# Kernel tuning notes

Hardware: AMD Instinct MI355X
Metric: run time of the kernel (lower is better)

## Reference

```python
import jax, jax.numpy as jnp
import numpy as np

B, N, D = 8, 256, 128
EPS_AGG = 1e-6
LN_EPS = 1e-5


def setup_inputs() -> dict:
    key = jax.random.key(0)
    ks = jax.random.split(key, 12)
    s = lambda fan_in: 1.0 / np.sqrt(fan_in)
    inp = {
        "x": jax.random.normal(ks[0], (B, N, D), dtype=jnp.float32),
        "edge0": jax.random.normal(ks[1], (B, N, N, D), dtype=jnp.float32),
        "edge_mask": jax.random.randint(ks[2], (B, N, N), 0, 2, dtype=jnp.int32),
        # msg_mlp: Linear(3D->D), ReLU, Linear(D->D)
        "W1m": jax.random.uniform(ks[3], (3 * D, D), jnp.float32, -s(3 * D), s(3 * D)),
        "b1m": jax.random.uniform(ks[4], (D,), jnp.float32, -s(3 * D), s(3 * D)),
        "W2m": jax.random.uniform(ks[5], (D, D), jnp.float32, -s(D), s(D)),
        "b2m": jax.random.uniform(ks[6], (D,), jnp.float32, -s(D), s(D)),
        # upd_mlp: Linear(2D->D), ReLU, Linear(D->D)
        "W1u": jax.random.uniform(ks[7], (2 * D, D), jnp.float32, -s(2 * D), s(2 * D)),
        "b1u": jax.random.uniform(ks[8], (D,), jnp.float32, -s(2 * D), s(2 * D)),
        "W2u": jax.random.uniform(ks[9], (D, D), jnp.float32, -s(D), s(D)),
        "b2u": jax.random.uniform(ks[10], (D,), jnp.float32, -s(D), s(D)),
        # LayerNorm affine
        "gamma": jnp.ones((D,), jnp.float32),
        "beta": jnp.zeros((D,), jnp.float32),
    }
    return inp


def reference(x, edge0, edge_mask, W1m, b1m, W2m, b2m, W1u, b1u, W2u, b2u, gamma, beta):
    # All-pairs concat: [B, N_i, N_j, 3D]
    xi = jnp.broadcast_to(x[:, :, None, :], (B, N, N, D))
    xj = jnp.broadcast_to(x[:, None, :, :], (B, N, N, D))
    msg_in = jnp.concatenate([xi, xj, edge0], axis=-1)
    # 2-layer edge MLP
    h = jax.nn.relu(jnp.einsum("bijk,kd->bijd", msg_in, W1m) + b1m)
    msg = jnp.einsum("bijk,kd->bijd", h, W2m) + b2m
    # mask + mean-style aggregation over neighbors j
    m = edge_mask.astype(jnp.float32)
    agg = jnp.einsum("bijd,bij->bid", msg, m) / (m.sum(axis=2, keepdims=True) + EPS_AGG)
    # update MLP
    u_in = jnp.concatenate([x, agg], axis=-1)  # [B, N, 2D]
    hu = jax.nn.relu(u_in @ W1u + b1u)
    out = hu @ W2u + b2u
    # residual + LayerNorm
    y = x + out
    mu = y.mean(axis=-1, keepdims=True)
    var = y.var(axis=-1, keepdims=True)
    return (y - mu) * jax.lax.rsqrt(var + LN_EPS) * gamma + beta
```

## Files before the change

kernel.cpp:

```cpp
#include <hip/hip_runtime.h>
#include <hip/hip_bf16.h>

typedef float    f4    __attribute__((ext_vector_type(4)));
typedef short    s8v   __attribute__((ext_vector_type(8)));
typedef __bf16   bf8v  __attribute__((ext_vector_type(8)));
typedef unsigned int u32x4v __attribute__((ext_vector_type(4)));
typedef unsigned short u16;

typedef const __attribute__((address_space(1))) void GAS;
typedef __attribute__((address_space(3))) void LAS;

#define NB 8
#define NN 256
#define ND 128

static __device__ __forceinline__ u16 f2bf(float f) {
    union { float f; unsigned u; } v; v.f = f;
    unsigned r = v.u + 0x7FFF + ((v.u >> 16) & 1);
    return (u16)(r >> 16);
}

static __device__ __forceinline__ unsigned pack2bf(float a, float b) {
    unsigned ua = __builtin_bit_cast(unsigned, a) + 0x8000u;
    unsigned ub = __builtin_bit_cast(unsigned, b) + 0x8000u;
    return __builtin_amdgcn_perm(ub, ua, 0x07060302u);
}

__global__ __launch_bounds__(256) void prep_kernel(
    const float* __restrict__ x, const float* __restrict__ W1m,
    const float* __restrict__ b1m,
    float* __restrict__ P, float* __restrict__ Qn, u16* __restrict__ W1cp)
{
    if (blockIdx.x == 1024) {
        for (int idx = threadIdx.x; idx < 16384; idx += 256) {
            int e  = idx & 7;
            int ln = (idx >> 3) & 63;
            int nt = (idx >> 9) & 7;
            int kt = idx >> 12;
            int k  = kt * 32 + (ln >> 4) * 8 + e;
            int d  = nt * 16 + (ln & 15);
            W1cp[idx] = f2bf(W1m[(2 * ND + k) * ND + d]);
        }
        return;
    }
    __shared__ float xl[256];
    int t = threadIdx.x;
    int row0 = blockIdx.x * 2;
    xl[t] = x[row0 * ND + t];
    __syncthreads();
    int r = t >> 7;
    int d = t & 127;
    int row = row0 + r;
    float sp = b1m[d], sq = 0.f;
    const float* xr = &xl[r * ND];
    #pragma unroll 8
    for (int k = 0; k < ND; ++k) {
        float xv = xr[k];
        sp += xv * W1m[k * ND + d];
        sq += xv * W1m[(ND + k) * ND + d];
    }
    P[row * ND + d] = sp;
    Qn[row * ND + d] = sq;
}

__global__ __launch_bounds__(256, 5) void fused_kernel(
    const float* __restrict__ x, const float* __restrict__ edge0,
    const int* __restrict__ mask,
    const float* __restrict__ W2m, const float* __restrict__ b2m,
    const float* __restrict__ W1u, const float* __restrict__ b1u,
    const float* __restrict__ W2u, const float* __restrict__ b2u,
    const float* __restrict__ gamma, const float* __restrict__ beta,
    const float* __restrict__ P, const float* __restrict__ Qn,
    const u16* __restrict__ W1cp,
    float* __restrict__ out)
{
    __shared__ float ebuf[3][2048];
    __shared__ float ml[NN];
    __shared__ float xrow[ND];
    __shared__ float redc[4], redA[4], redB[4];

    float* aggH = &ebuf[1][0];
    float* am   = &ebuf[1][128];
    float* hu   = &ebuf[1][256];
    float* yl   = &ebuf[1][384];

    const int bid  = (blockIdx.x & 7) * 256 + (blockIdx.x >> 3);
    const int b    = bid >> 8;
    const int tid  = threadIdx.x;
    const int wave = tid >> 6;
    const int lane = tid & 63;
    const int l15  = lane & 15;
    const int lg   = lane >> 4;

    const char* e0c = (const char*)(edge0 + (size_t)bid * (NN * ND));

    float mval = (float)mask[bid * NN + tid];
    ml[tid] = mval;
    if (tid < ND) xrow[tid] = x[bid * ND + tid];

    s8v bfr[4][2];
    #pragma unroll
    for (int kt = 0; kt < 4; ++kt)
        #pragma unroll
        for (int n = 0; n < 2; ++n)
            bfr[kt][n] = *reinterpret_cast<const s8v*>(
                &W1cp[(((kt * 8) + (wave * 2 + n)) * 64 + lane) * 8]);

    const int col0 = wave * 32 + l15;
    const float pv0 = P[bid * ND + col0];
    const float pv1 = P[bid * ND + col0 + 16];
    const float* qbase = Qn + ((size_t)b * NN + lg * 4) * ND + col0;

    auto STAGE = [&](int cc, int bb) {
        const char* cb = e0c + (size_t)cc * 8192;
        #pragma unroll
        for (int u = 0; u < 2; ++u) {
            int row  = wave * 4 + u * 2 + (lane >> 5);
            int colb = (lane & 31) * 16;
            const char* g = cb + row * 512 + (colb ^ ((row & 7) << 4));
            __builtin_amdgcn_global_load_lds(
                (GAS*)g, (LAS*)&ebuf[bb][(wave * 2 + u) * 256], 16, 0, 0);
        }
    };

    float q0v[2][4], q1v[2][4];
    auto LOADQ = [&](int cc, int gg) {
        const float* qr = qbase + (size_t)cc * 16 * ND;
        #pragma unroll
        for (int r = 0; r < 4; ++r) {
            q0v[gg][r] = qr[r * ND];
            q1v[gg][r] = qr[r * ND + 16];
        }
    };

    float agg0 = 0.f, agg1 = 0.f;

    asm volatile("s_waitcnt vmcnt(0) lgkmcnt(0)" ::: "memory");
    __builtin_amdgcn_sched_barrier(0);
    STAGE(0, 0);
    __builtin_amdgcn_sched_barrier(0);
    LOADQ(0, 0);
    __builtin_amdgcn_sched_barrier(0);
    STAGE(1, 1);
    __builtin_amdgcn_sched_barrier(0);

    #pragma unroll
    for (int c = 0; c < 16; ++c) {
        if (c < 15)
            asm volatile("s_waitcnt vmcnt(10) lgkmcnt(0)" ::: "memory");
        else
            asm volatile("s_waitcnt vmcnt(8) lgkmcnt(0)" ::: "memory");
        __builtin_amdgcn_s_barrier();
        __builtin_amdgcn_sched_barrier(0);
        if (c < 15) {
            LOADQ(c + 1, (c + 1) & 1);
            __builtin_amdgcn_sched_barrier(0);
            if (c < 14) {
                STAGE(c + 2, (c + 2) % 3);
                __builtin_amdgcn_sched_barrier(0);
            }
        }
        const char* bufc = (const char*)&ebuf[c % 3][0];
        const int rb  = l15 * 512;
        const int swz = (l15 & 7) << 4;
        f4 acc0 = {0.f, 0.f, 0.f, 0.f};
        f4 acc1 = {0.f, 0.f, 0.f, 0.f};
        #pragma unroll
        for (int kt = 0; kt < 4; ++kt) {
            int cbyte = kt * 128 + lg * 32;
            f4 a0 = *reinterpret_cast<const f4*>(bufc + rb + ((cbyte)      ^ swz));
            f4 a1 = *reinterpret_cast<const f4*>(bufc + rb + ((cbyte + 16) ^ swz));
            u32x4v aw;
            aw[0] = pack2bf(a0[0], a0[1]);
            aw[1] = pack2bf(a0[2], a0[3]);
            aw[2] = pack2bf(a1[0], a1[1]);
            aw[3] = pack2bf(a1[2], a1[3]);
            bf8v av = __builtin_bit_cast(bf8v, aw);
            acc0 = __builtin_amdgcn_mfma_f32_16x16x32_bf16(
                av, __builtin_bit_cast(bf8v, bfr[kt][0]), acc0, 0, 0, 0);
            acc1 = __builtin_amdgcn_mfma_f32_16x16x32_bf16(
                av, __builtin_bit_cast(bf8v, bfr[kt][1]), acc1, 0, 0, 0);
        }
        f4 mk = *reinterpret_cast<const f4*>(&ml[c * 16 + lg * 4]);
        const int g = c & 1;
        #pragma unroll
        for (int r = 0; r < 4; ++r) {
            float h0 = fmaxf(acc0[r] + pv0 + q0v[g][r], 0.f);
            float h1 = fmaxf(acc1[r] + pv1 + q1v[g][r], 0.f);
            agg0 += mk[r] * h0;
            agg1 += mk[r] * h1;
        }
    }

    agg0 += __shfl_xor(agg0, 16); agg0 += __shfl_xor(agg0, 32);
    agg1 += __shfl_xor(agg1, 16); agg1 += __shfl_xor(agg1, 32);
    if (lg == 0) {
        aggH[wave * 32 + l15]      = agg0;
        aggH[wave * 32 + 16 + l15] = agg1;
    }
    float cv = mval;
    #pragma unroll
    for (int o = 32; o > 0; o >>= 1) cv += __shfl_xor(cv, o);
    if (lane == 0) redc[wave] = cv;
    __syncthreads();

    const float cnt = redc[0] + redc[1] + redc[2] + redc[3];
    const float inv = 1.f / (cnt + 1e-6f);
    const int d  = tid & 127;
    const int hf = tid >> 7;

    {
        float s = 0.f;
        #pragma unroll 8
        for (int k = hf * 64; k < hf * 64 + 64; ++k) s += aggH[k] * W2m[k * ND + d];
        ml[tid] = s;
    }
    __syncthreads();
    if (tid < ND) am[d] = (ml[d] + ml[d + ND] + cnt * b2m[d]) * inv;
    __syncthreads();
    {
        float s = 0.f;
        const float* W = W1u + (size_t)hf * ND * ND;
        const float* v = hf ? am : xrow;
        #pragma unroll 8
        for (int k = 0; k < ND; ++k) s += v[k] * W[k * ND + d];
        ml[tid] = s;
    }
    __syncthreads();
    if (tid < ND) hu[d] = fmaxf(ml[d] + ml[d + ND] + b1u[d], 0.f);
    __syncthreads();
    {
        float s = 0.f;
        #pragma unroll 8
        for (int k = hf * 64; k < hf * 64 + 64; ++k) s += hu[k] * W2u[k * ND + d];
        ml[tid] = s;
    }
    __syncthreads();
    if (tid < ND) yl[d] = xrow[d] + ml[d] + ml[d + ND] + b2u[d];
    __syncthreads();
    float yv = (tid < ND) ? yl[tid] : 0.f;
    float s1 = yv, s2 = yv * yv;
    #pragma unroll
    for (int o = 32; o > 0; o >>= 1) { s1 += __shfl_xor(s1, o); s2 += __shfl_xor(s2, o); }
    if (lane == 0) { redA[wave] = s1; redB[wave] = s2; }
    __syncthreads();
    if (tid < ND) {
        float mu  = (redA[0] + redA[1] + redA[2] + redA[3]) * (1.f / 128.f);
        float ex2 = (redB[0] + redB[1] + redB[2] + redB[3]) * (1.f / 128.f);
        float var = ex2 - mu * mu;
        float rs  = rsqrtf(var + 1e-5f);
        out[bid * ND + d] = (yl[d] - mu) * rs * gamma[d] + beta[d];
    }
}

extern "C" void kernel_launch(void* const* d_in, const int* in_sizes, int n_in,
                              void* d_out, int out_size, void* d_ws, size_t ws_size,
                              hipStream_t stream) {
    (void)in_sizes; (void)n_in; (void)out_size; (void)ws_size;
    const float* x     = (const float*)d_in[0];
    const float* edge0 = (const float*)d_in[1];
    const int*   mask  = (const int*)d_in[2];
    const float* W1m   = (const float*)d_in[3];
    const float* b1m   = (const float*)d_in[4];
    const float* W2m   = (const float*)d_in[5];
    const float* b2m   = (const float*)d_in[6];
    const float* W1u   = (const float*)d_in[7];
    const float* b1u   = (const float*)d_in[8];
    const float* W2u   = (const float*)d_in[9];
    const float* b2u   = (const float*)d_in[10];
    const float* gamma = (const float*)d_in[11];
    const float* beta  = (const float*)d_in[12];

    float* P    = (float*)d_ws;
    float* Qn   = P + 2048 * 128;
    u16*   W1cp = (u16*)(Qn + 2048 * 128);

    float* o = (float*)d_out;

    prep_kernel<<<dim3(1025), dim3(256), 0, stream>>>(x, W1m, b1m, P, Qn, W1cp);
    fused_kernel<<<dim3(2048), dim3(256), 0, stream>>>(
        x, edge0, mask, W2m, b2m, W1u, b1u, W2u, b2u, gamma, beta,
        P, Qn, W1cp, o);
}
```

Measured before the change: 95.60 us.

## Stage edge tiles through registers and store them as bf16 in LDS

Measured after the change: 82.11 us. 14.1% less time.

```diff
diff --git a/kernel.cpp b/kernel.cpp
--- a/kernel.cpp
+++ b/kernel.cpp
@@ -6,9 +6,6 @@
 typedef __bf16   bf8v  __attribute__((ext_vector_type(8)));
 typedef unsigned int u32x4v __attribute__((ext_vector_type(4)));
 typedef unsigned short u16;
-
-typedef const __attribute__((address_space(1))) void GAS;
-typedef __attribute__((address_space(3))) void LAS;
 
 #define NB 8
 #define NN 256
@@ -74,7 +71,7 @@
     const u16* __restrict__ W1cp,
     float* __restrict__ out)
 {
-    __shared__ float ebuf[3][2048];
+    __shared__ float ebuf[3][1024];
     __shared__ float ml[NN];
     __shared__ float xrow[ND];
     __shared__ float redc[4], redA[4], redB[4];
@@ -111,97 +108,95 @@
     const float pv1 = P[bid * ND + col0 + 16];
     const float* qbase = Qn + ((size_t)b * NN + lg * 4) * ND + col0;
 
-    auto STAGE = [&](int cc, int bb) {
-        const char* cb = e0c + (size_t)cc * 8192;
-        #pragma unroll
-        for (int u = 0; u < 2; ++u) {
-            int row  = wave * 4 + u * 2 + (lane >> 5);
-            int colb = (lane & 31) * 16;
-            const char* g = cb + row * 512 + (colb ^ ((row & 7) << 4));
-            __builtin_amdgcn_global_load_lds(
-                (GAS*)g, (LAS*)&ebuf[bb][(wave * 2 + u) * 256], 16, 0, 0);
-        }
+    const int srow  = tid >> 4;
+    const int swoff = srow * 256 + (((tid & 15) * 16) ^ ((srow & 7) << 4));
+
+    auto LOADE = [&](int cc, f4* er) {
+        const char* cb = e0c + (size_t)cc * 8192 + tid * 32;
+        er[0] = *reinterpret_cast<const f4*>(cb);
+        er[1] = *reinterpret_cast<const f4*>(cb + 16);
     };
-
-    float q0v[2][4], q1v[2][4];
-    auto LOADQ = [&](int cc, int gg) {
-        const float* qr = qbase + (size_t)cc * 16 * ND;
-        #pragma unroll
-        for (int r = 0; r < 4; ++r) {
-            q0v[gg][r] = qr[r * ND];
-            q1v[gg][r] = qr[r * ND + 16];
-        }
+    auto WRITEE = [&](const f4* er, int bb) {
+        u32x4v aw;
+        aw[0] = pack2bf(er[0][0], er[0][1]);
+        aw[1] = pack2bf(er[0][2], er[0][3]);
+        aw[2] = pack2bf(er[1][0], er[1][1]);
+        aw[3] = pack2bf(er[1][2], er[1][3]);
+        *reinterpret_cast<u32x4v*>(
+            reinterpret_cast<char*>(&ebuf[bb][0]) + swoff) = aw;
     };
 
     float agg0 = 0.f, agg1 = 0.f;
-
-    asm volatile("s_waitcnt vmcnt(0) lgkmcnt(0)" ::: "memory");
+    f4 eA[2], eB[2];
+
+    LOADE(0, eA);
     __builtin_amdgcn_sched_barrier(0);
-    STAGE(0, 0);
+    LOADE(1, eB);
     __builtin_amdgcn_sched_barrier(0);
-    LOADQ(0, 0);
-    __builtin_amdgcn_sched_barrier(0);
-    STAGE(1, 1);
-    __builtin_amdgcn_sched_barrier(0);
+    asm volatile("s_waitcnt vmcnt(2)" ::: "memory");
+    WRITEE(eA, 0);
+    asm volatile("s_waitcnt lgkmcnt(0)" ::: "memory");
 
     #pragma unroll
     for (int c = 0; c < 16; ++c) {
-        if (c < 15)
-            asm volatile("s_waitcnt vmcnt(10) lgkmcnt(0)" ::: "memory");
-        else
-            asm volatile("s_waitcnt vmcnt(8) lgkmcnt(0)" ::: "memory");
         __builtin_amdgcn_s_barrier();
         __builtin_amdgcn_sched_barrier(0);
-        if (c < 15) {
-            LOADQ(c + 1, (c + 1) & 1);
+        float q0v[4], q1v[4];
+        {
+            const float* qr = qbase + (size_t)c * 16 * ND;
+            #pragma unroll
+            for (int r = 0; r < 4; ++r) {
+                q0v[r] = qr[r * ND];
+                q1v[r] = qr[r * ND + 16];
+            }
+        }
+        __builtin_amdgcn_sched_barrier(0);
+        if (c < 14) {
+            if (c & 1) LOADE(c + 2, eA); else LOADE(c + 2, eB);
             __builtin_amdgcn_sched_barrier(0);
-            if (c < 14) {
-                STAGE(c + 2, (c + 2) % 3);
-                __builtin_amdgcn_sched_barrier(0);
-            }
         }
         const char* bufc = (const char*)&ebuf[c % 3][0];
-        const int rb  = l15 * 512;
+        const int rb  = l15 * 256;
         const int swz = (l15 & 7) << 4;
         f4 acc0 = {0.f, 0.f, 0.f, 0.f};
         f4 acc1 = {0.f, 0.f, 0.f, 0.f};
         #pragma unroll
         for (int kt = 0; kt < 4; ++kt) {
-            int cbyte = kt * 128 + lg * 32;
-            f4 a0 = *reinterpret_cast<const f4*>(bufc + rb + ((cbyte)      ^ swz));
-            f4 a1 = *reinterpret_cast<const f4*>(bufc + rb + ((cbyte + 16) ^ swz));
-            u32x4v aw;
-            aw[0] = pack2bf(a0[0], a0[1]);
-            aw[1] = pack2bf(a0[2], a0[3]);
-            aw[2] = pack2bf(a1[0], a1[1]);
-            aw[3] = pack2bf(a1[2], a1[3]);
-            bf8v av = __builtin_bit_cast(bf8v, aw);
+            s8v av = *reinterpret_cast<const s8v*>(
+                bufc + rb + ((kt * 64 + lg * 16) ^ swz));
             acc0 = __builtin_amdgcn_mfma_f32_16x16x32_bf16(
-                av, __builtin_bit_cast(bf8v, bfr[kt][0]), acc0, 0, 0, 0);
+                __builtin_bit_cast(bf8v, av), __builtin_bit_cast(bf8v, bfr[kt][0]), acc0, 0, 0, 0);
             acc1 = __builtin_amdgcn_mfma_f32_16x16x32_bf16(
-                av, __builtin_bit_cast(bf8v, bfr[kt][1]), acc1, 0, 0, 0);
+                __builtin_bit_cast(bf8v, av), __builtin_bit_cast(bf8v, bfr[kt][1]), acc1, 0, 0, 0);
         }
         f4 mk = *reinterpret_cast<const f4*>(&ml[c * 16 + lg * 4]);
-        const int g = c & 1;
         #pragma unroll
         for (int r = 0; r < 4; ++r) {
-            float h0 = fmaxf(acc0[r] + pv0 + q0v[g][r], 0.f);
-            float h1 = fmaxf(acc1[r] + pv1 + q1v[g][r], 0.f);
+            float h0 = fmaxf(acc0[r] + pv0 + q0v[r], 0.f);
+            float h1 = fmaxf(acc1[r] + pv1 + q1v[r], 0.f);
             agg0 += mk[r] * h0;
             agg1 += mk[r] * h1;
         }
+        __builtin_amdgcn_sched_barrier(0);
+        if (c < 15) {
+            asm volatile("s_waitcnt vmcnt(2)" ::: "memory");
+            if (c & 1) WRITEE(eA, (c + 1) % 3); else WRITEE(eB, (c + 1) % 3);
+            asm volatile("s_waitcnt lgkmcnt(0)" ::: "memory");
+            __builtin_amdgcn_sched_barrier(0);
+        }
     }
 
     agg0 += __shfl_xor(agg0, 16); agg0 += __shfl_xor(agg0, 32);
     agg1 += __shfl_xor(agg1, 16); agg1 += __shfl_xor(agg1, 32);
+    float cv = mval;
+    #pragma unroll
+    for (int o = 32; o > 0; o >>= 1) cv += __shfl_xor(cv, o);
+    if (lane == 0) redc[wave] = cv;
+    __syncthreads();
     if (lg == 0) {
         aggH[wave * 32 + l15]      = agg0;
         aggH[wave * 32 + 16 + l15] = agg1;
     }
-    float cv = mval;
-    #pragma unroll
-    for (int o = 32; o > 0; o >>= 1) cv += __shfl_xor(cv, o);
-    if (lane == 0) redc[wave] = cv;
     __syncthreads();
 
     const float cnt = redc[0] + redc[1] + redc[2] + redc[3];
```

## Split fused kernel into per-wave edge kernel and batched node tail kernel

Applied to the files above, without the earlier changes.

After: 128.9 us. 1.35x slower.

```diff
diff --git a/kernel.cpp b/kernel.cpp
--- a/kernel.cpp
+++ b/kernel.cpp
@@ -5,6 +5,7 @@
 typedef short    s8v   __attribute__((ext_vector_type(8)));
 typedef __bf16   bf8v  __attribute__((ext_vector_type(8)));
 typedef unsigned int u32x4v __attribute__((ext_vector_type(4)));
+typedef int      i4    __attribute__((ext_vector_type(4)));
 typedef unsigned short u16;
 
 typedef const __attribute__((address_space(1))) void GAS;
@@ -13,6 +14,7 @@
 #define NB 8
 #define NN 256
 #define ND 128
+#define SB0() __builtin_amdgcn_sched_barrier(0)
 
 static __device__ __forceinline__ u16 f2bf(float f) {
     union { float f; unsigned u; } v; v.f = f;
@@ -29,7 +31,7 @@
 __global__ __launch_bounds__(256) void prep_kernel(
     const float* __restrict__ x, const float* __restrict__ W1m,
     const float* __restrict__ b1m,
-    float* __restrict__ P, float* __restrict__ Qn, u16* __restrict__ W1cp)
+    float* __restrict__ P, float* __restrict__ Qp2, u16* __restrict__ W1cp)
 {
     if (blockIdx.x == 1024) {
         for (int idx = threadIdx.x; idx < 16384; idx += 256) {
@@ -48,11 +50,11 @@
     int row0 = blockIdx.x * 2;
     xl[t] = x[row0 * ND + t];
     __syncthreads();
-    int r = t >> 7;
+    int r2 = t >> 7;
     int d = t & 127;
-    int row = row0 + r;
+    int row = row0 + r2;
     float sp = b1m[d], sq = 0.f;
-    const float* xr = &xl[r * ND];
+    const float* xr = &xl[r2 * ND];
     #pragma unroll 8
     for (int k = 0; k < ND; ++k) {
         float xv = xr[k];
@@ -60,43 +62,36 @@
         sq += xv * W1m[(ND + k) * ND + d];
     }
     P[row * ND + d] = sp;
-    Qn[row * ND + d] = sq;
-}
-
-__global__ __launch_bounds__(256, 5) void fused_kernel(
-    const float* __restrict__ x, const float* __restrict__ edge0,
-    const int* __restrict__ mask,
-    const float* __restrict__ W2m, const float* __restrict__ b2m,
-    const float* __restrict__ W1u, const float* __restrict__ b1u,
-    const float* __restrict__ W2u, const float* __restrict__ b2u,
-    const float* __restrict__ gamma, const float* __restrict__ beta,
-    const float* __restrict__ P, const float* __restrict__ Qn,
+    int b   = row >> 8;
+    int j   = row & 255;
+    int gc  = j >> 4;
+    int lgq = (j & 15) >> 2;
+    int r   = j & 3;
+    int colq = d >> 5;
+    int half = (d >> 4) & 1;
+    int lane = lgq * 16 + (d & 15);
+    Qp2[((((size_t)b * 16 + gc) * 4 + colq) * 64 + lane) * 8 + half * 4 + r] = sq;
+}
+
+__global__ __launch_bounds__(64, 4) void edge_kernel(
+    const float* __restrict__ edge0, const int* __restrict__ mask,
+    const float* __restrict__ P, const float* __restrict__ Qp2,
     const u16* __restrict__ W1cp,
-    float* __restrict__ out)
+    float* __restrict__ aggP)
 {
-    __shared__ float ebuf[3][2048];
-    __shared__ float ml[NN];
-    __shared__ float xrow[ND];
-    __shared__ float redc[4], redA[4], redB[4];
-
-    float* aggH = &ebuf[1][0];
-    float* am   = &ebuf[1][128];
-    float* hu   = &ebuf[1][256];
-    float* yl   = &ebuf[1][384];
-
-    const int bid  = (blockIdx.x & 7) * 256 + (blockIdx.x >> 3);
-    const int b    = bid >> 8;
-    const int tid  = threadIdx.x;
-    const int wave = tid >> 6;
-    const int lane = tid & 63;
+    __shared__ float ebuf[2][2048];
+
+    const int b    = blockIdx.x & 7;
+    const int k    = blockIdx.x >> 3;
+    const int i    = k >> 2;
+    const int colq = k & 3;
+    const int bid  = b * 256 + i;
+
+    const int lane = threadIdx.x;
     const int l15  = lane & 15;
     const int lg   = lane >> 4;
 
     const char* e0c = (const char*)(edge0 + (size_t)bid * (NN * ND));
-
-    float mval = (float)mask[bid * NN + tid];
-    ml[tid] = mval;
-    if (tid < ND) xrow[tid] = x[bid * ND + tid];
 
     s8v bfr[4][2];
     #pragma unroll
@@ -104,67 +99,50 @@
         #pragma unroll
         for (int n = 0; n < 2; ++n)
             bfr[kt][n] = *reinterpret_cast<const s8v*>(
-                &W1cp[(((kt * 8) + (wave * 2 + n)) * 64 + lane) * 8]);
-
-    const int col0 = wave * 32 + l15;
+                &W1cp[(((kt * 8) + (colq * 2 + n)) * 64 + lane) * 8]);
+
+    const int col0 = colq * 32 + l15;
     const float pv0 = P[bid * ND + col0];
     const float pv1 = P[bid * ND + col0 + 16];
-    const float* qbase = Qn + ((size_t)b * NN + lg * 4) * ND + col0;
 
     auto STAGE = [&](int cc, int bb) {
         const char* cb = e0c + (size_t)cc * 8192;
         #pragma unroll
-        for (int u = 0; u < 2; ++u) {
-            int row  = wave * 4 + u * 2 + (lane >> 5);
+        for (int u = 0; u < 8; ++u) {
+            int row  = u * 2 + (lane >> 5);
             int colb = (lane & 31) * 16;
             const char* g = cb + row * 512 + (colb ^ ((row & 7) << 4));
             __builtin_amdgcn_global_load_lds(
-                (GAS*)g, (LAS*)&ebuf[bb][(wave * 2 + u) * 256], 16, 0, 0);
+                (GAS*)g, (LAS*)&ebuf[bb][u * 256], 16, 0, 0);
         }
     };
-
-    float q0v[2][4], q1v[2][4];
-    auto LOADQ = [&](int cc, int gg) {
-        const float* qr = qbase + (size_t)cc * 16 * ND;
-        #pragma unroll
-        for (int r = 0; r < 4; ++r) {
-            q0v[gg][r] = qr[r * ND];
-            q1v[gg][r] = qr[r * ND + 16];
-        }
+    f4 qg[2][2];
+    i4 mg[2];
+    auto LOADQM = [&](int cc, int g) {
+        const f4* qp = reinterpret_cast<const f4*>(
+            Qp2 + ((((size_t)b * 16 + cc) * 4 + colq) * 64 + lane) * 8);
+        qg[g][0] = qp[0];
+        qg[g][1] = qp[1];
+        mg[g] = *reinterpret_cast<const i4*>(mask + bid * NN + cc * 16 + lg * 4);
     };
 
     float agg0 = 0.f, agg1 = 0.f;
 
-    asm volatile("s_waitcnt vmcnt(0) lgkmcnt(0)" ::: "memory");
-    __builtin_amdgcn_sched_barrier(0);
-    STAGE(0, 0);
-    __builtin_amdgcn_sched_barrier(0);
-    LOADQ(0, 0);
-    __builtin_amdgcn_sched_barrier(0);
-    STAGE(1, 1);
-    __builtin_amdgcn_sched_barrier(0);
+    STAGE(0, 0); SB0();
+    LOADQM(0, 0); SB0();
+    STAGE(1, 1); SB0();
 
     #pragma unroll
     for (int c = 0; c < 16; ++c) {
-        if (c < 15)
-            asm volatile("s_waitcnt vmcnt(10) lgkmcnt(0)" ::: "memory");
-        else
-            asm volatile("s_waitcnt vmcnt(8) lgkmcnt(0)" ::: "memory");
-        __builtin_amdgcn_s_barrier();
-        __builtin_amdgcn_sched_barrier(0);
-        if (c < 15) {
-            LOADQ(c + 1, (c + 1) & 1);
-            __builtin_amdgcn_sched_barrier(0);
-            if (c < 14) {
-                STAGE(c + 2, (c + 2) % 3);
-                __builtin_amdgcn_sched_barrier(0);
-            }
-        }
-        const char* bufc = (const char*)&ebuf[c % 3][0];
+        const int cur = c & 1;
+        if (c < 15) { LOADQM(c + 1, cur ^ 1); SB0(); }
+        if (c < 15) asm volatile("s_waitcnt vmcnt(14)" ::: "memory");
+        else        asm volatile("s_waitcnt vmcnt(3)"  ::: "memory");
+        SB0();
+        const char* bufc = (const char*)&ebuf[cur][0];
         const int rb  = l15 * 512;
         const int swz = (l15 & 7) << 4;
-        f4 acc0 = {0.f, 0.f, 0.f, 0.f};
-        f4 acc1 = {0.f, 0.f, 0.f, 0.f};
+        s8v apk[4];
         #pragma unroll
         for (int kt = 0; kt < 4; ++kt) {
             int cbyte = kt * 128 + lg * 32;
@@ -175,81 +153,151 @@
             aw[1] = pack2bf(a0[2], a0[3]);
             aw[2] = pack2bf(a1[0], a1[1]);
             aw[3] = pack2bf(a1[2], a1[3]);
-            bf8v av = __builtin_bit_cast(bf8v, aw);
+            apk[kt] = __builtin_bit_cast(s8v, aw);
+        }
+        asm volatile("s_waitcnt lgkmcnt(0)" ::: "memory");
+        SB0();
+        if (c < 14) { STAGE(c + 2, cur); SB0(); }
+        f4 acc0 = {0.f, 0.f, 0.f, 0.f};
+        f4 acc1 = {0.f, 0.f, 0.f, 0.f};
+        #pragma unroll
+        for (int kt = 0; kt < 4; ++kt) {
             acc0 = __builtin_amdgcn_mfma_f32_16x16x32_bf16(
-                av, __builtin_bit_cast(bf8v, bfr[kt][0]), acc0, 0, 0, 0);
+                __builtin_bit_cast(bf8v, apk[kt]), __builtin_bit_cast(bf8v, bfr[kt][0]), acc0, 0, 0, 0);
             acc1 = __builtin_amdgcn_mfma_f32_16x16x32_bf16(
-                av, __builtin_bit_cast(bf8v, bfr[kt][1]), acc1, 0, 0, 0);
-        }
-        f4 mk = *reinterpret_cast<const f4*>(&ml[c * 16 + lg * 4]);
-        const int g = c & 1;
+                __builtin_bit_cast(bf8v, apk[kt]), __builtin_bit_cast(bf8v, bfr[kt][1]), acc1, 0, 0, 0);
+        }
         #pragma unroll
         for (int r = 0; r < 4; ++r) {
-            float h0 = fmaxf(acc0[r] + pv0 + q0v[g][r], 0.f);
-            float h1 = fmaxf(acc1[r] + pv1 + q1v[g][r], 0.f);
-            agg0 += mk[r] * h0;
-            agg1 += mk[r] * h1;
+            float mk = (float)mg[cur][r];
+            float h0 = fmaxf(acc0[r] + pv0 + qg[cur][0][r], 0.f);
+            float h1 = fmaxf(acc1[r] + pv1 + qg[cur][1][r], 0.f);
+            agg0 += mk * h0;
+            agg1 += mk * h1;
         }
     }
 
     agg0 += __shfl_xor(agg0, 16); agg0 += __shfl_xor(agg0, 32);
     agg1 += __shfl_xor(agg1, 16); agg1 += __shfl_xor(agg1, 32);
     if (lg == 0) {
-        aggH[wave * 32 + l15]      = agg0;
-        aggH[wave * 32 + 16 + l15] = agg1;
-    }
-    float cv = mval;
-    #pragma unroll
-    for (int o = 32; o > 0; o >>= 1) cv += __shfl_xor(cv, o);
-    if (lane == 0) redc[wave] = cv;
-    __syncthreads();
-
-    const float cnt = redc[0] + redc[1] + redc[2] + redc[3];
-    const float inv = 1.f / (cnt + 1e-6f);
+        aggP[(size_t)bid * ND + col0]      = agg0;
+        aggP[(size_t)bid * ND + col0 + 16] = agg1;
+    }
+}
+
+__global__ __launch_bounds__(256) void tail_kernel(
+    const float* __restrict__ x, const int* __restrict__ mask,
+    const float* __restrict__ aggP,
+    const float* __restrict__ W2m, const float* __restrict__ b2m,
+    const float* __restrict__ W1u, const float* __restrict__ b1u,
+    const float* __restrict__ W2u, const float* __restrict__ b2u,
+    const float* __restrict__ gamma, const float* __restrict__ beta,
+    float* __restrict__ out)
+{
+    __shared__ float ah[8][ND], xr[8][ND], am[8][ND], hu[8][ND], yl[8][ND];
+    __shared__ float cl[8];
+    const int tid = threadIdx.x;
+    const int blk = blockIdx.x;
+
+    {
+        const f4* sa = reinterpret_cast<const f4*>(aggP + (size_t)blk * 1024);
+        const f4* sx = reinterpret_cast<const f4*>(x + (size_t)blk * 1024);
+        reinterpret_cast<f4*>(&ah[0][0])[tid] = sa[tid];
+        reinterpret_cast<f4*>(&xr[0][0])[tid] = sx[tid];
+    }
+    {
+        int node = tid >> 5, t32 = tid & 31;
+        const int* mrow = mask + ((size_t)blk * 8 + node) * NN;
+        int s = 0;
+        #pragma unroll
+        for (int jj = 0; jj < 8; ++jj) s += mrow[t32 + jj * 32];
+        s += __shfl_xor(s, 16); s += __shfl_xor(s, 8);
+        s += __shfl_xor(s, 4);  s += __shfl_xor(s, 2); s += __shfl_xor(s, 1);
+        if (t32 == 0) cl[node] = (float)s;
+    }
+    __syncthreads();
+
     const int d  = tid & 127;
-    const int hf = tid >> 7;
-
-    {
-        float s = 0.f;
-        #pragma unroll 8
-        for (int k = hf * 64; k < hf * 64 + 64; ++k) s += aggH[k] * W2m[k * ND + d];
-        ml[tid] = s;
-    }
-    __syncthreads();
-    if (tid < ND) am[d] = (ml[d] + ml[d + ND] + cnt * b2m[d]) * inv;
-    __syncthreads();
-    {
-        float s = 0.f;
-        const float* W = W1u + (size_t)hf * ND * ND;
-        const float* v = hf ? am : xrow;
-        #pragma unroll 8
-        for (int k = 0; k < ND; ++k) s += v[k] * W[k * ND + d];
-        ml[tid] = s;
-    }
-    __syncthreads();
-    if (tid < ND) hu[d] = fmaxf(ml[d] + ml[d + ND] + b1u[d], 0.f);
-    __syncthreads();
-    {
-        float s = 0.f;
-        #pragma unroll 8
-        for (int k = hf * 64; k < hf * 64 + 64; ++k) s += hu[k] * W2u[k * ND + d];
-        ml[tid] = s;
-    }
-    __syncthreads();
-    if (tid < ND) yl[d] = xrow[d] + ml[d] + ml[d + ND] + b2u[d];
-    __syncthreads();
-    float yv = (tid < ND) ? yl[tid] : 0.f;
-    float s1 = yv, s2 = yv * yv;
-    #pragma unroll
-    for (int o = 32; o > 0; o >>= 1) { s1 += __shfl_xor(s1, o); s2 += __shfl_xor(s2, o); }
-    if (lane == 0) { redA[wave] = s1; redB[wave] = s2; }
-    __syncthreads();
-    if (tid < ND) {
-        float mu  = (redA[0] + redA[1] + redA[2] + redA[3]) * (1.f / 128.f);
-        float ex2 = (redB[0] + redB[1] + redB[2] + redB[3]) * (1.f / 128.f);
-        float var = ex2 - mu * mu;
-        float rs  = rsqrtf(var + 1e-5f);
-        out[bid * ND + d] = (yl[d] - mu) * rs * gamma[d] + beta[d];
+    const int ng = tid >> 7;
+
+    {
+        float s0 = 0.f, s1 = 0.f, s2 = 0.f, s3 = 0.f;
+        #pragma unroll 4
+        for (int kk = 0; kk < ND; ++kk) {
+            float w = W2m[kk * ND + d];
+            s0 += ah[ng * 4 + 0][kk] * w;
+            s1 += ah[ng * 4 + 1][kk] * w;
+            s2 += ah[ng * 4 + 2][kk] * w;
+            s3 += ah[ng * 4 + 3][kk] * w;
+        }
+        float bb = b2m[d];
+        am[ng * 4 + 0][d] = (s0 + cl[ng * 4 + 0] * bb) / (cl[ng * 4 + 0] + 1e-6f);
+        am[ng * 4 + 1][d] = (s1 + cl[ng * 4 + 1] * bb) / (cl[ng * 4 + 1] + 1e-6f);
+        am[ng * 4 + 2][d] = (s2 + cl[ng * 4 + 2] * bb) / (cl[ng * 4 + 2] + 1e-6f);
+        am[ng * 4 + 3][d] = (s3 + cl[ng * 4 + 3] * bb) / (cl[ng * 4 + 3] + 1e-6f);
+    }
+    __syncthreads();
+    {
+        float bb = b1u[d];
+        float s0 = bb, s1 = bb, s2 = bb, s3 = bb;
+        #pragma unroll 4
+        for (int kk = 0; kk < ND; ++kk) {
+            float w = W1u[kk * ND + d];
+            s0 += xr[ng * 4 + 0][kk] * w;
+            s1 += xr[ng * 4 + 1][kk] * w;
+            s2 += xr[ng * 4 + 2][kk] * w;
+            s3 += xr[ng * 4 + 3][kk] * w;
+        }
+        #pragma unroll 4
+        for (int kk = 0; kk < ND; ++kk) {
+            float w = W1u[(ND + kk) * ND + d];
+            s0 += am[ng * 4 + 0][kk] * w;
+            s1 += am[ng * 4 + 1][kk] * w;
+            s2 += am[ng * 4 + 2][kk] * w;
+            s3 += am[ng * 4 + 3][kk] * w;
+        }
+        hu[ng * 4 + 0][d] = fmaxf(s0, 0.f);
+        hu[ng * 4 + 1][d] = fmaxf(s1, 0.f);
+        hu[ng * 4 + 2][d] = fmaxf(s2, 0.f);
+        hu[ng * 4 + 3][d] = fmaxf(s3, 0.f);
+    }
+    __syncthreads();
+    {
+        float bb = b2u[d];
+        float s0 = bb, s1 = bb, s2 = bb, s3 = bb;
+        #pragma unroll 4
+        for (int kk = 0; kk < ND; ++kk) {
+            float w = W2u[kk * ND + d];
+            s0 += hu[ng * 4 + 0][kk] * w;
+            s1 += hu[ng * 4 + 1][kk] * w;
+            s2 += hu[ng * 4 + 2][kk] * w;
+            s3 += hu[ng * 4 + 3][kk] * w;
+        }
+        yl[ng * 4 + 0][d] = xr[ng * 4 + 0][d] + s0;
+        yl[ng * 4 + 1][d] = xr[ng * 4 + 1][d] + s1;
+        yl[ng * 4 + 2][d] = xr[ng * 4 + 2][d] + s2;
+        yl[ng * 4 + 3][d] = xr[ng * 4 + 3][d] + s3;
+    }
+    __syncthreads();
+    {
+        int node = tid >> 5, t32 = tid & 31;
+        f4 v = *reinterpret_cast<const f4*>(&yl[node][t32 * 4]);
+        float s1 = v[0] + v[1] + v[2] + v[3];
+        float s2 = v[0]*v[0] + v[1]*v[1] + v[2]*v[2] + v[3]*v[3];
+        s1 += __shfl_xor(s1, 16); s2 += __shfl_xor(s2, 16);
+        s1 += __shfl_xor(s1, 8);  s2 += __shfl_xor(s2, 8);
+        s1 += __shfl_xor(s1, 4);  s2 += __shfl_xor(s2, 4);
+        s1 += __shfl_xor(s1, 2);  s2 += __shfl_xor(s2, 2);
+        s1 += __shfl_xor(s1, 1);  s2 += __shfl_xor(s2, 1);
+        float mu  = s1 * (1.f / 128.f);
+        float ex2 = s2 * (1.f / 128.f);
+        float rs  = rsqrtf(ex2 - mu * mu + 1e-5f);
+        float* orow = out + ((size_t)blk * 8 + node) * ND + t32 * 4;
+        #pragma unroll
+        for (int e = 0; e < 4; ++e) {
+            int dd = t32 * 4 + e;
+            orow[e] = (v[e] - mu) * rs * gamma[dd] + beta[dd];
+        }
     }
 }
 
@@ -272,13 +320,14 @@
     const float* beta  = (const float*)d_in[12];
 
     float* P    = (float*)d_ws;
-    float* Qn   = P + 2048 * 128;
-    u16*   W1cp = (u16*)(Qn + 2048 * 128);
+    float* Qp2  = P + 2048 * 128;
+    u16*   W1cp = (u16*)(Qp2 + 2048 * 128);
+    float* aggP = (float*)(W1cp + 16384);
 
     float* o = (float*)d_out;
 
-    prep_kernel<<<dim3(1025), dim3(256), 0, stream>>>(x, W1m, b1m, P, Qn, W1cp);
-    fused_kernel<<<dim3(2048), dim3(256), 0, stream>>>(
-        x, edge0, mask, W2m, b2m, W1u, b1u, W2u, b2u, gamma, beta,
-        P, Qn, W1cp, o);
-}
+    prep_kernel<<<dim3(1025), dim3(256), 0, stream>>>(x, W1m, b1m, P, Qp2, W1cp);
+    edge_kernel<<<dim3(8192), dim3(64), 0, stream>>>(edge0, mask, P, Qp2, W1cp, aggP);
+    tail_kernel<<<dim3(256), dim3(256), 0, stream>>>(
+        x, mask, aggP, W2m, b2m, W1u, b1u, W2u, b2u, gamma, beta, o);
+}
```
